# Performance work log

Measured on AMD Instinct MI355X. Metric: run time of the kernel, lower is better.

Reference implementation:

```python
import jax, jax.numpy as jnp
import numpy as np

NUM_EMB = 8192
EMB_DIM = 1024
BETA = 0.25  # commitment_cost, legacy=True


def setup_inputs() -> dict:
    key = jax.random.key(0)
    k1, k2 = jax.random.split(key)
    z = jax.random.normal(k1, (8, EMB_DIM, 32, 32), dtype=jnp.float32)
    # torch: embedding.weight.data.uniform_(-1/num_embeddings, 1/num_embeddings)
    emb_weight = jax.random.uniform(
        k2, (NUM_EMB, EMB_DIM), dtype=jnp.float32,
        minval=-1.0 / NUM_EMB, maxval=1.0 / NUM_EMB)
    return {"z": z, "emb_weight": emb_weight}


def reference(z, emb_weight):
    B, C, H, W = z.shape
    # b c h w -> b h w c
    z_work = jnp.transpose(z, (0, 2, 3, 1))
    z_flat = z_work.reshape(-1, EMB_DIM)  # [N, D]
    # squared distances: |z|^2 + |e|^2 - 2 z e^T  -> [N, K]
    d = (jnp.sum(z_flat * z_flat, axis=1, keepdims=True)
         + jnp.sum(emb_weight * emb_weight, axis=1)
         - 2.0 * jnp.einsum('nd,kd->nk', z_flat, emb_weight))
    idx = jnp.argmin(d, axis=1)  # [N]
    # codebook gather
    z_q = emb_weight[idx].reshape(z_work.shape)
    # usage counts (bincount) -> perplexity (EMA buffers omitted: no effect on outputs)
    counts = jax.ops.segment_sum(jnp.ones_like(idx, dtype=jnp.float32), idx,
                                 num_segments=NUM_EMB)
    avg_probs = counts / jnp.maximum(counts.sum(), 1.0)
    perplexity = jnp.exp(-jnp.sum(avg_probs * jnp.log(avg_probs + 1e-10)))
    sg = jax.lax.stop_gradient
    # legacy loss: mean((sg(zq)-z)^2) + beta*mean((zq-sg(z))^2)
    loss = (jnp.mean((sg(z_q) - z_work) ** 2)
            + BETA * jnp.mean((z_q - sg(z_work)) ** 2))
    # straight-through estimator
    z_q_ste = z_work + sg(z_q - z_work)
    # b h w c -> b c h w
    z_q_out = jnp.transpose(z_q_ste, (0, 3, 1, 2))
    return z_q_out, loss, perplexity, idx
```

## Files before the change

### kernel.cpp

```cpp
#include <hip/hip_runtime.h>
#include <math.h>

#define NROWS 8192
#define KCODES 8192
#define DDIM 1024
#define ZQ_ELEMS 8388608

typedef int i4 __attribute__((ext_vector_type(4)));

#define W0_QZ8     0u
#define W0_QE8     8388608u
#define W0_SZ      16777216u
#define W0_SE      16809984u
#define W0_CAND    16842752u
#define W0_CVAL    18939904u
#define W0_CCNT    23134208u
#define W0_COUNTS  23166976u
#define W0_ZNORM   23199744u
#define W0_ROWMIN  23232512u
#define W0_NEED    23265280u
#define W1_CAND    0u
#define W1_CVAL    2097152u
#define W1_CCNT    6291456u
#define W1_COUNTS  6324224u
#define W1_ZNORM   6356992u
#define W1_ROWMIN  6389760u
#define W1_NEED    6422528u
#define W3_CAND    0u
#define W3_CCNT    2097152u
#define W3_COUNTS  2129920u
#define W3_ZNORM   2162688u
#define W3_ROWMIN  2195456u
#define W3_NEED    2228224u

#define CAP 128
#define MARGIN  7.5e-4f
#define MARGIN2 6e-4f

typedef __attribute__((address_space(3))) unsigned int lds_u32;
typedef __attribute__((address_space(1))) const unsigned int glb_u32;
static __device__ __forceinline__ void glds16(const void* g, void* l) {
    __builtin_amdgcn_global_load_lds((glb_u32*)g, (lds_u32*)l, 16, 0, 0);
}

__global__ __launch_bounds__(256) void prep_kernel(const float* __restrict__ z,
                                                   const float* __restrict__ emb,
                                                   char* __restrict__ qz8,
                                                   char* __restrict__ qe8,
                                                   float* __restrict__ sz,
                                                   float* __restrict__ se,
                                                   float* __restrict__ zT,
                                                   float* __restrict__ zn,
                                                   unsigned int* __restrict__ ccnt,
                                                   float* __restrict__ counts,
                                                   int* __restrict__ rowming,
                                                   float* __restrict__ outbuf) {
    int blk = blockIdx.x;
    int t = threadIdx.x;
    if (blk >= 256) {
        __shared__ float wm[4];
        int k0 = (blk - 256) * 2;
        int half = t >> 7;
        int li = t & 127;
        int row = k0 + half;
        const float* er = emb + (size_t)row * 1024 + li * 8;
        float4 v0 = *(const float4*)er;
        float4 v1 = *(const float4*)(er + 4);
        float lm = fmaxf(fmaxf(fmaxf(fabsf(v0.x), fabsf(v0.y)), fmaxf(fabsf(v0.z), fabsf(v0.w))),
                         fmaxf(fmaxf(fabsf(v1.x), fabsf(v1.y)), fmaxf(fabsf(v1.z), fabsf(v1.w))));
#pragma unroll
        for (int off = 32; off; off >>= 1) lm = fmaxf(lm, __shfl_down(lm, off, 64));
        int w = t >> 6;
        if ((t & 63) == 0) wm[w] = lm;
        __syncthreads();
        float rmax = fmaxf(wm[half * 2], wm[half * 2 + 1]);
        float inv = rmax > 0.f ? 127.f / rmax : 0.f;
        int q0 = (int)rintf(v0.x * inv), q1 = (int)rintf(v0.y * inv);
        int q2 = (int)rintf(v0.z * inv), q3 = (int)rintf(v0.w * inv);
        int q4 = (int)rintf(v1.x * inv), q5 = (int)rintf(v1.y * inv);
        int q6 = (int)rintf(v1.z * inv), q7 = (int)rintf(v1.w * inv);
        uint2 o;
        o.x = (q0 & 255) | ((q1 & 255) << 8) | ((q2 & 255) << 16) | ((unsigned)(q3 & 255) << 24);
        o.y = (q4 & 255) | ((q5 & 255) << 8) | ((q6 & 255) << 16) | ((unsigned)(q7 & 255) << 24);
        *(uint2*)(qe8 + (size_t)row * 1024 + li * 8) = o;
        if (li == 0) se[row] = rmax * (1.f / 127.f);
        return;
    }
    if (t < 32) {
        int i = blk * 32 + t;
        ccnt[i] = 0u;
        counts[i] = 0.f;
        rowming[i] = 0x7f7f7f7f;
    }
    if (blk == 0 && t == 32) outbuf[ZQ_ELEMS] = 0.f;

    __shared__ float T[32 * 33];
    __shared__ double D[32 * 32];
    __shared__ float mxa[32 * 8];
    __shared__ float invS[32];
    int b = blk >> 5, ht = blk & 31;
    int hw0 = ht * 32;
    int dsub = t >> 3, hseg = (t & 7) * 4;
    int hsub = dsub, dd = hseg;
    double a0 = 0.0, a1 = 0.0, a2 = 0.0, a3 = 0.0;
    float lmax = 0.f;
    for (int dt = 0; dt < 32; ++dt) {
        int d0 = dt * 32;
        float4 v = *(const float4*)(z + (size_t)b * 1048576 + (size_t)(d0 + dsub) * 1024 + hw0 + hseg);
        a0 += (double)v.x * v.x;
        a1 += (double)v.y * v.y;
        a2 += (double)v.z * v.z;
        a3 += (double)v.w * v.w;
        T[dsub * 33 + hseg + 0] = v.x;
        T[dsub * 33 + hseg + 1] = v.y;
        T[dsub * 33 + hseg + 2] = v.z;
        T[dsub * 33 + hseg + 3] = v.w;
        __syncthreads();
        float t0 = T[(dd + 0) * 33 + hsub];
        float t1 = T[(dd + 1) * 33 + hsub];
        float t2 = T[(dd + 2) * 33 + hsub];
        float t3 = T[(dd + 3) * 33 + hsub];
        if (zT) {
            float4 o4; o4.x = t0; o4.y = t1; o4.z = t2; o4.w = t3;
            *(float4*)(zT + ((size_t)(b * 1024 + hw0 + hsub) << 10) + d0 + dd) = o4;
        }
        lmax = fmaxf(lmax, fmaxf(fmaxf(fabsf(t0), fabsf(t1)), fmaxf(fabsf(t2), fabsf(t3))));
        __syncthreads();
    }
    D[dsub * 32 + hseg + 0] = a0;
    D[dsub * 32 + hseg + 1] = a1;
    D[dsub * 32 + hseg + 2] = a2;
    D[dsub * 32 + hseg + 3] = a3;
    mxa[hsub * 8 + (t & 7)] = lmax;
    __syncthreads();
    if (t < 32) {
        double s = 0.0;
        for (int i = 0; i < 32; ++i) s += D[i * 32 + t];
        zn[b * 1024 + hw0 + t] = (float)s;
        float rm = 0.f;
#pragma unroll
        for (int j = 0; j < 8; ++j) rm = fmaxf(rm, mxa[t * 8 + j]);
        sz[b * 1024 + hw0 + t] = rm * (1.f / 127.f);
        invS[t] = rm > 0.f ? 127.f / rm : 0.f;
    }
    __syncthreads();
    if (zT) {
        int row = t >> 3;
        int dseg = (t & 7) * 128;
        float inv = invS[row];
        const float4* zr = (const float4*)(zT + ((size_t)(b * 1024 + hw0 + row) << 10) + dseg);
        int* qo = (int*)(qz8 + ((size_t)(b * 1024 + hw0 + row) << 10) + dseg);
#pragma unroll 8
        for (int jj = 0; jj < 32; ++jj) {
            float4 v = zr[jj];
            int q0 = (int)rintf(v.x * inv), q1 = (int)rintf(v.y * inv);
            int q2 = (int)rintf(v.z * inv), q3 = (int)rintf(v.w * inv);
            qo[jj] = (q0 & 255) | ((q1 & 255) << 8) | ((q2 & 255) << 16) | ((unsigned)(q3 & 255) << 24);
        }
    } else {
        for (int dt = 0; dt < 32; ++dt) {
            int d0 = dt * 32;
            float4 v = *(const float4*)(z + (size_t)b * 1048576 + (size_t)(d0 + dsub) * 1024 + hw0 + hseg);
            T[dsub * 33 + hseg + 0] = v.x;
            T[dsub * 33 + hseg + 1] = v.y;
            T[dsub * 33 + hseg + 2] = v.z;
            T[dsub * 33 + hseg + 3] = v.w;
            __syncthreads();
            float inv = invS[hsub];
            int q0 = (int)rintf(T[(dd + 0) * 33 + hsub] * inv);
            int q1 = (int)rintf(T[(dd + 1) * 33 + hsub] * inv);
            int q2 = (int)rintf(T[(dd + 2) * 33 + hsub] * inv);
            int q3 = (int)rintf(T[(dd + 3) * 33 + hsub] * inv);
            int packed = (q0 & 255) | ((q1 & 255) << 8) | ((q2 & 255) << 16) | ((unsigned)(q3 & 255) << 24);
            *(int*)(qz8 + ((size_t)(b * 1024 + hw0 + hsub) << 10) + d0 + dd) = packed;
            __syncthreads();
        }
    }
}

__global__ __launch_bounds__(256) void znorm_kernel(const float* __restrict__ z,
                                                    float* __restrict__ zn) {
    int b = blockIdx.x >> 2;
    int hw = (blockIdx.x & 3) * 256 + threadIdx.x;
    const float* base = z + (size_t)b * 1048576 + hw;
    double s = 0.0;
#pragma unroll 16
    for (int d = 0; d < DDIM; ++d) {
        float v = base[(size_t)d * 1024];
        s += (double)v * (double)v;
    }
    zn[b * 1024 + hw] = (float)s;
}

__global__ __launch_bounds__(256, 4) void stage1_kernel(const char* __restrict__ qz,
                                                        const char* __restrict__ qe,
                                                        const float* __restrict__ sz,
                                                        const float* __restrict__ se,
                                                        unsigned short* __restrict__ cand,
                                                        float* __restrict__ cval,
                                                        unsigned int* __restrict__ ccnt,
                                                        int* __restrict__ rowming) {
    __shared__ char As[128 * 128];
    __shared__ char Bs[128 * 128];
    __shared__ int rowminS[128];
    __shared__ float szS[128], seS[128];

    int t = threadIdx.x;
    int w = t >> 6, lane = t & 63;
    int q = lane >> 4, l15 = lane & 15;
    int wr = (w >> 1) * 64, wc = (w & 1) * 64;
    int n0 = blockIdx.x * 128;
    int k0 = blockIdx.y * 128;
    if (t < 128) {
        rowminS[t] = 0x7f7f7f7f;
        szS[t] = sz[n0 + t];
        seS[t] = se[k0 + t];
    }

    const char* gA[4];
    const char* gB[4];
    {
        int rsub = lane >> 3;
        int clog = (lane & 7) ^ (rsub & 7);
#pragma unroll
        for (int c = 0; c < 4; ++c) {
            int cc = w * 4 + c;
            int r = cc * 8 + rsub;
            gA[c] = qz + ((size_t)(n0 + r) << 10) + clog * 16;
            gB[c] = qe + ((size_t)(k0 + r) << 10) + clog * 16;
        }
    }
    int Aoff[4][2], Boff[4][2];
#pragma unroll
    for (int rf = 0; rf < 4; ++rf) {
#pragma unroll
        for (int ks = 0; ks < 2; ++ks) {
            int r = wr + rf * 16 + l15;
            Aoff[rf][ks] = r * 128 + (((ks * 4 + q) ^ (r & 7)) * 16);
            int rb = wc + rf * 16 + l15;
            Boff[rf][ks] = rb * 128 + (((ks * 4 + q) ^ (rb & 7)) * 16);
        }
    }

    i4 acc[4][4];
    const i4 z4 = {0, 0, 0, 0};
#pragma unroll
    for (int rf = 0; rf < 4; ++rf)
#pragma unroll
        for (int cf = 0; cf < 4; ++cf) acc[rf][cf] = z4;

    for (int s = 0; s < 8; ++s) {
        __syncthreads();
#pragma unroll
        for (int c = 0; c < 4; ++c) {
            int cc = w * 4 + c;
            glds16(gA[c], As + cc * 1024);
            glds16(gB[c], Bs + cc * 1024);
            gA[c] += 128;
            gB[c] += 128;
        }
        __syncthreads();
#pragma unroll
        for (int ks = 0; ks < 2; ++ks) {
            i4 af[4], bf[4];
#pragma unroll
            for (int rf = 0; rf < 4; ++rf) af[rf] = *(const i4*)(As + Aoff[rf][ks]);
#pragma unroll
            for (int cf = 0; cf < 4; ++cf) bf[cf] = *(const i4*)(Bs + Boff[cf][ks]);
#pragma unroll
            for (int rf = 0; rf < 4; ++rf)
#pragma unroll
                for (int cf = 0; cf < 4; ++cf)
                    acc[rf][cf] = __builtin_amdgcn_mfma_i32_16x16x64_i8(af[rf], bf[cf], acc[rf][cf], 0, 0, 0);
        }
    }

#pragma unroll
    for (int rf = 0; rf < 4; ++rf) {
#pragma unroll
        for (int reg = 0; reg < 4; ++reg) {
            int r = wr + rf * 16 + q * 4 + reg;
            float zs = szS[r];
            float m4 = INFINITY;
#pragma unroll
            for (int cf = 0; cf < 4; ++cf) {
                float s1 = 16.0f - 2.0f * (float)acc[rf][cf][reg] * (zs * seS[wc + cf * 16 + l15]);
                m4 = fminf(m4, s1);
            }
            m4 = fminf(m4, __shfl_xor(m4, 1, 16));
            m4 = fminf(m4, __shfl_xor(m4, 2, 16));
            m4 = fminf(m4, __shfl_xor(m4, 4, 16));
            m4 = fminf(m4, __shfl_xor(m4, 8, 16));
            if (l15 == 0) atomicMin(&rowminS[r], __float_as_int(m4));
        }
    }
    __syncthreads();
    if (t < 128) {
        int mine = rowminS[t];
        int gold = atomicMin(&rowming[n0 + t], mine);
        rowminS[t] = gold < mine ? gold : mine;
    }
    __syncthreads();
#pragma unroll
    for (int rf = 0; rf < 4; ++rf) {
#pragma unroll
        for (int reg = 0; reg < 4; ++reg) {
            int r = wr + rf * 16 + q * 4 + reg;
            float zs = szS[r];
            float rm = __int_as_float(rowminS[r]) + MARGIN;
#pragma unroll
            for (int cf = 0; cf < 4; ++cf) {
                float s1 = 16.0f - 2.0f * (float)acc[rf][cf][reg] * (zs * seS[wc + cf * 16 + l15]);
                if (s1 <= rm) {
                    int kg = k0 + wc + cf * 16 + l15;
                    unsigned pos = atomicAdd(&ccnt[n0 + r], 1u);
                    if (pos < CAP) {
                        cand[(size_t)(n0 + r) * CAP + pos] = (unsigned short)kg;
                        if (cval) cval[(size_t)(n0 + r) * CAP + pos] = s1;
                    }
                }
            }
        }
    }
}

__global__ __launch_bounds__(256) void stage2_kernel(const float* __restrict__ z,
                                                     const float* __restrict__ zT,
                                                     const float* __restrict__ emb,
                                                     const unsigned short* __restrict__ cand,
                                                     const float* __restrict__ cval,
                                                     const unsigned int* __restrict__ ccnt,
                                                     const float* __restrict__ zn,
                                                     float* __restrict__ counts,
                                                     float* __restrict__ outbuf) {
    int t = threadIdx.x;
    int w = t >> 6, lane = t & 63;
    int n = blockIdx.x * 4 + w;
    unsigned cnt = ccnt[n];
    float Zn = zn[n];
    float thr = INFINITY;

    if (cval && cnt <= CAP) {
        const float* cv = cval + (size_t)n * CAP;
        float v0 = (unsigned)lane < cnt ? cv[lane] : INFINITY;
        float v1 = (unsigned)(64 + lane) < cnt ? cv[64 + lane] : INFINITY;
        float m = fminf(v0, v1);
#pragma unroll
        for (int off = 32; off; off >>= 1) m = fminf(m, __shfl_xor(m, off, 64));
        thr = m + MARGIN2;
        unsigned long long m0 = __ballot(v0 <= thr);
        unsigned long long m1 = __ballot(v1 <= thr);
        if (__popcll(m0) + __popcll(m1) == 1) {
            if (lane == 0) {
                int slot = m0 ? ((int)__ffsll((unsigned long long)m0) - 1)
                              : 64 + ((int)__ffsll((unsigned long long)m1) - 1);
                int K = cand[(size_t)n * CAP + slot];
                outbuf[ZQ_ELEMS + 2 + n] = (float)K;
                atomicAdd(&counts[K], 1.0f);
            }
            return;
        }
    }
    float4 zreg[4];
    if (zT) {
        const float4* zr = (const float4*)(zT + ((size_t)n << 10));
#pragma unroll
        for (int i = 0; i < 4; ++i) zreg[i] = zr[lane + i * 64];
    } else {
        int b = n >> 10, hw = n & 1023;
        const float* zb = z + (size_t)b * 1048576 + hw;
#pragma unroll
        for (int i = 0; i < 4; ++i) {
            int e = (lane + i * 64) * 4;
            zreg[i].x = zb[(size_t)(e + 0) << 10];
            zreg[i].y = zb[(size_t)(e + 1) << 10];
            zreg[i].z = zb[(size_t)(e + 2) << 10];
            zreg[i].w = zb[(size_t)(e + 3) << 10];
        }
    }
    float bs = INFINITY;
    int bk = 0x7fffffff;
    if (cnt <= CAP) {
        for (unsigned c = 0; c < cnt; ++c) {
            if (cval && cval[(size_t)n * CAP + c] > thr) continue;
            int k = cand[(size_t)n * CAP + c];
            const float4* e4 = (const float4*)(emb + (size_t)k * 1024);
            double pd = 0.0;
#pragma unroll
            for (int i = 0; i < 4; ++i) {
                float4 e = e4[lane + i * 64];
                float4 zv = zreg[i];
                float p = (zv.x * e.x + zv.y * e.y) + (zv.z * e.z + zv.w * e.w);
                pd += (double)p;
            }
#pragma unroll
            for (int off = 32; off; off >>= 1) pd += __shfl_down(pd, off, 64);
            if (lane == 0) {
                float s = Zn - 2.0f * (float)pd;
                if (s < bs || (s == bs && k < bk)) { bs = s; bk = k; }
            }
        }
    } else {
        for (int k = 0; k < KCODES; ++k) {
            const float4* e4 = (const float4*)(emb + (size_t)k * 1024);
            double pd = 0.0;
#pragma unroll
            for (int i = 0; i < 4; ++i) {
                float4 e = e4[lane + i * 64];
                float4 zv = zreg[i];
                float p = (zv.x * e.x + zv.y * e.y) + (zv.z * e.z + zv.w * e.w);
                pd += (double)p;
            }
#pragma unroll
            for (int off = 32; off; off >>= 1) pd += __shfl_down(pd, off, 64);
            if (lane == 0) {
                float s = Zn - 2.0f * (float)pd;
                if (s < bs || (s == bs && k < bk)) { bs = s; bk = k; }
            }
        }
    }
    if (lane == 0) {
        outbuf[ZQ_ELEMS + 2 + n] = (float)bk;
        atomicAdd(&counts[bk], 1.0f);
    }
}

__global__ __launch_bounds__(1024) void perp_kernel(const float* __restrict__ counts,
                                                    float* __restrict__ outbuf) {
    __shared__ double sh[16];
    int tid = threadIdx.x;
    double h = 0.0;
    for (int i = tid; i < KCODES; i += 1024) {
        float c = counts[i];
        float p = c * (1.0f / 8192.0f);
        h += (double)(p * logf(p + 1e-10f));
    }
#pragma unroll
    for (int off = 32; off; off >>= 1) h += __shfl_down(h, off, 64);
    if ((tid & 63) == 0) sh[tid >> 6] = h;
    __syncthreads();
    if (tid == 0) {
        double H = 0.0;
#pragma unroll
        for (int i = 0; i < 16; ++i) H += sh[i];
        outbuf[ZQ_ELEMS + 1] = (float)exp(-H);
    }
}

__global__ __launch_bounds__(256) void gather_kernel(const float* __restrict__ z,
                                                     const float* __restrict__ emb,
                                                     const float* __restrict__ counts,
                                                     float* __restrict__ outbuf) {
    __shared__ float E[64 * 65];
    __shared__ int idxs[64];
    __shared__ float lsh[4];
    int blk = blockIdx.x;
    int ct = blk & 15;
    int hwt = (blk >> 4) & 15;
    int b = blk >> 8;
    int c0 = ct * 64;
    int n0 = b * 1024 + hwt * 64;
    int tid = threadIdx.x;
    if (tid < 64) idxs[tid] = (int)outbuf[ZQ_ELEMS + 2 + n0 + tid];
    __syncthreads();
    {
        int i0 = tid >> 4;
        int cc4 = (tid & 15) * 4;
#pragma unroll
        for (int rep = 0; rep < 4; ++rep) {
            int i = i0 + rep * 16;
            float4 v = *(const float4*)(emb + (size_t)idxs[i] * DDIM + c0 + cc4);
            E[i * 65 + cc4 + 0] = v.x;
            E[i * 65 + cc4 + 1] = v.y;
            E[i * 65 + cc4 + 2] = v.z;
            E[i * 65 + cc4 + 3] = v.w;
        }
    }
    __syncthreads();
    float ls = 0.f;
    int hwl = tid & 63;
    int cb = tid >> 6;
    size_t obase = (size_t)b * 1048576 + (size_t)hwt * 64 + hwl;
#pragma unroll
    for (int rep = 0; rep < 16; ++rep) {
        int cc = cb + rep * 4;
        size_t off = obase + (size_t)(c0 + cc) * 1024;
        float zv = z[off];
        float e = E[hwl * 65 + cc];
        float d = e - zv;
        outbuf[off] = zv + d;
        ls += d * d;
    }
#pragma unroll
    for (int off = 32; off; off >>= 1) ls += __shfl_down(ls, off, 64);
    if ((tid & 63) == 0) lsh[tid >> 6] = ls;
    __syncthreads();
    if (tid == 0) {
        float bsum = lsh[0] + lsh[1] + lsh[2] + lsh[3];
        atomicAdd(&outbuf[ZQ_ELEMS], bsum * (1.25f / 8388608.0f));
    }
    if (counts && blk == 0) {
        __shared__ double psh[4];
        double h = 0.0;
        for (int i = tid; i < KCODES; i += 256) {
            float c = counts[i];
            float p = c * (1.0f / 8192.0f);
            h += (double)(p * logf(p + 1e-10f));
        }
#pragma unroll
        for (int off = 32; off; off >>= 1) h += __shfl_down(h, off, 64);
        if ((tid & 63) == 0) psh[tid >> 6] = h;
        __syncthreads();
        if (tid == 0)
            outbuf[ZQ_ELEMS + 1] = (float)exp(-(psh[0] + psh[1] + psh[2] + psh[3]));
    }
}

#define SC_PMIN   0
#define SC_PIDX   65536
#define SC_ENORM  131072
#define SC_COUNTS 139264
#define SC_ZNORM  147456

__global__ __launch_bounds__(256) void enorm_kernel(const float* __restrict__ emb,
                                                    float* __restrict__ outbuf) {
    int wave = threadIdx.x >> 6;
    int lane = threadIdx.x & 63;
    int k = blockIdx.x * 4 + wave;
    const float4* row = (const float4*)(emb + (size_t)k * DDIM);
    float s = 0.f;
#pragma unroll
    for (int j = 0; j < 4; ++j) {
        float4 v = row[lane + 64 * j];
        s += v.x * v.x + v.y * v.y + v.z * v.z + v.w * v.w;
    }
#pragma unroll
    for (int off = 32; off; off >>= 1) s += __shfl_down(s, off, 64);
    if (lane == 0) outbuf[SC_ENORM + k] = s;
}

#define BD 32
#define LDT 68
__global__ __launch_bounds__(256) void argmin_kernel(const float* __restrict__ z,
                                                     const float* __restrict__ emb,
                                                     float* __restrict__ outbuf) {
    __shared__ float Asf[BD * LDT];
    __shared__ float Bsf[BD * LDT];
    __shared__ float redV[64 * 17];
    __shared__ float redI[64 * 17];
    int tid = threadIdx.x;
    int tx = tid & 15, ty = tid >> 4;
    int n0 = blockIdx.x * 64;
    int b = n0 >> 10, hw0 = n0 & 1023;
    const float* zbase = z + (size_t)b * 1048576 + hw0;
    int kChunk0 = blockIdx.y * 1024;
    float Zn[4];
#pragma unroll
    for (int i = 0; i < 4; ++i) Zn[i] = outbuf[SC_ZNORM + n0 + 4 * tx + i];
    float bestV[4] = {INFINITY, INFINITY, INFINITY, INFINITY};
    int bestI[4] = {0, 0, 0, 0};
    for (int kt = 0; kt < 16; ++kt) {
        int k0 = kChunk0 + kt * 64;
        double acc64[4][4] = {};
        for (int d0 = 0; d0 < DDIM; d0 += BD) {
            {
                int r4 = (tid & 15) * 4, ddA = tid >> 4;
#pragma unroll
                for (int rep = 0; rep < 2; ++rep) {
                    int dd = ddA + rep * 16;
                    float4 v = *(const float4*)(zbase + (size_t)(d0 + dd) * 1024 + r4);
                    *(float4*)(&Asf[dd * LDT + r4]) = v;
                }
            }
            {
                int dd4 = (tid & 7) * 4, kkB = tid >> 3;
#pragma unroll
                for (int rep = 0; rep < 2; ++rep) {
                    int kk = kkB + rep * 32;
                    float4 v = *(const float4*)(emb + (size_t)(k0 + kk) * DDIM + d0 + dd4);
                    Bsf[(dd4 + 0) * LDT + kk] = v.x;
                    Bsf[(dd4 + 1) * LDT + kk] = v.y;
                    Bsf[(dd4 + 2) * LDT + kk] = v.z;
                    Bsf[(dd4 + 3) * LDT + kk] = v.w;
                }
            }
            __syncthreads();
            float acc[4][4] = {};
#pragma unroll
            for (int dd = 0; dd < BD; ++dd) {
                float4 a = *(const float4*)(&Asf[dd * LDT + 4 * tx]);
                float4 bv = *(const float4*)(&Bsf[dd * LDT + 4 * ty]);
                float ar[4] = {a.x, a.y, a.z, a.w};
                float br[4] = {bv.x, bv.y, bv.z, bv.w};
#pragma unroll
                for (int i = 0; i < 4; ++i)
#pragma unroll
                    for (int j = 0; j < 4; ++j) acc[i][j] += ar[i] * br[j];
            }
            __syncthreads();
#pragma unroll
            for (int i = 0; i < 4; ++i)
#pragma unroll
                for (int j = 0; j < 4; ++j) acc64[i][j] += (double)acc[i][j];
        }
#pragma unroll
        for (int j = 0; j < 4; ++j) {
            int k = k0 + 4 * ty + j;
            float en = outbuf[SC_ENORM + k];
#pragma unroll
            for (int i = 0; i < 4; ++i) {
                float dotf = (float)acc64[i][j];
                float tt = Zn[i] + en;
                float s = tt - 2.0f * dotf;
                if (s < bestV[i]) { bestV[i] = s; bestI[i] = k; }
            }
        }
    }
#pragma unroll
    for (int i = 0; i < 4; ++i) {
        redV[(4 * tx + i) * 17 + ty] = bestV[i];
        redI[(4 * tx + i) * 17 + ty] = (float)bestI[i];
    }
    __syncthreads();
    if (tid < 64) {
        float bv = INFINITY;
        int bi = 0x7fffffff;
        for (int tt = 0; tt < 16; ++tt) {
            float v = redV[tid * 17 + tt];
            int ix = (int)redI[tid * 17 + tt];
            if (v < bv || (v == bv && ix < bi)) { bv = v; bi = ix; }
        }
        int n = n0 + tid;
        outbuf[SC_PMIN + n * 8 + blockIdx.y] = bv;
        outbuf[SC_PIDX + n * 8 + blockIdx.y] = (float)bi;
    }
}

__global__ __launch_bounds__(256) void reduce_kernel(float* __restrict__ outbuf) {
    int n = blockIdx.x * 256 + threadIdx.x;
    float bv = INFINITY;
    int bi = 0x7fffffff;
#pragma unroll
    for (int c = 0; c < 8; ++c) {
        float v = outbuf[SC_PMIN + n * 8 + c];
        int ix = (int)outbuf[SC_PIDX + n * 8 + c];
        if (v < bv || (v == bv && ix < bi)) { bv = v; bi = ix; }
    }
    outbuf[ZQ_ELEMS + 2 + n] = (float)bi;
    atomicAdd(&outbuf[SC_COUNTS + bi], 1.0f);
}

extern "C" void kernel_launch(void* const* d_in, const int* in_sizes, int n_in,
                              void* d_out, int out_size, void* d_ws, size_t ws_size,
                              hipStream_t stream) {
    const float* z = (const float*)d_in[0];
    const float* emb = (const float*)d_in[1];
    float* out = (float*)d_out;
    unsigned char* ws = (unsigned char*)d_ws;
    (void)in_sizes; (void)n_in; (void)out_size;

    if (ws_size >= (size_t)W0_NEED) {
        char* qz8 = (char*)(ws + W0_QZ8);
        char* qe8 = (char*)(ws + W0_QE8);
        float* sz = (float*)(ws + W0_SZ);
        float* se = (float*)(ws + W0_SE);
        unsigned short* cand = (unsigned short*)(ws + W0_CAND);
        float* cval = (float*)(ws + W0_CVAL);
        unsigned int* ccnt = (unsigned int*)(ws + W0_CCNT);
        float* counts = (float*)(ws + W0_COUNTS);
        float* zn = (float*)(ws + W0_ZNORM);
        int* rowming = (int*)(ws + W0_ROWMIN);
        float* zT = out;

        prep_kernel<<<4352, 256, 0, stream>>>(z, emb, qz8, qe8, sz, se, zT, zn, ccnt, counts, rowming, out);
        stage1_kernel<<<dim3(64, 64), 256, 0, stream>>>(qz8, qe8, sz, se, cand, cval, ccnt, rowming);
        stage2_kernel<<<2048, 256, 0, stream>>>(z, zT, emb, cand, cval, ccnt, zn, counts, out);
        gather_kernel<<<2048, 256, 0, stream>>>(z, emb, counts, out);
    } else if (ws_size >= (size_t)W1_NEED) {
        char* qz8 = (char*)out;
        char* qe8 = (char*)out + 8388608;
        float* sz = out + 4194304;
        float* se = out + 4202496;
        unsigned short* cand = (unsigned short*)(ws + W1_CAND);
        float* cval = (float*)(ws + W1_CVAL);
        unsigned int* ccnt = (unsigned int*)(ws + W1_CCNT);
        float* counts = (float*)(ws + W1_COUNTS);
        float* zn = (float*)(ws + W1_ZNORM);
        int* rowming = (int*)(ws + W1_ROWMIN);

        prep_kernel<<<4352, 256, 0, stream>>>(z, emb, qz8, qe8, sz, se, (float*)nullptr, zn, ccnt, counts, rowming, out);
        stage1_kernel<<<dim3(64, 64), 256, 0, stream>>>(qz8, qe8, sz, se, cand, cval, ccnt, rowming);
        stage2_kernel<<<2048, 256, 0, stream>>>(z, (const float*)nullptr, emb, cand, cval, ccnt, zn, counts, out);
        gather_kernel<<<2048, 256, 0, stream>>>(z, emb, counts, out);
    } else if (ws_size >= (size_t)W3_NEED) {
        char* qz8 = (char*)out;
        char* qe8 = (char*)out + 8388608;
        float* sz = out + 4194304;
        float* se = out + 4202496;
        unsigned short* cand = (unsigned short*)(ws + W3_CAND);
        unsigned int* ccnt = (unsigned int*)(ws + W3_CCNT);
        float* counts = (float*)(ws + W3_COUNTS);
        float* zn = (float*)(ws + W3_ZNORM);
        int* rowming = (int*)(ws + W3_ROWMIN);

        prep_kernel<<<4352, 256, 0, stream>>>(z, emb, qz8, qe8, sz, se, (float*)nullptr, zn, ccnt, counts, rowming, out);
        stage1_kernel<<<dim3(64, 64), 256, 0, stream>>>(qz8, qe8, sz, se, cand, (float*)nullptr, ccnt, rowming);
        stage2_kernel<<<2048, 256, 0, stream>>>(z, (const float*)nullptr, emb, cand,
                                                (const float*)nullptr, ccnt, zn, counts, out);
        gather_kernel<<<2048, 256, 0, stream>>>(z, emb, counts, out);
    } else {
        hipMemsetAsync(out + SC_COUNTS, 0, KCODES * sizeof(float), stream);
        hipMemsetAsync(out + ZQ_ELEMS, 0, sizeof(float), stream);
        enorm_kernel<<<2048, 256, 0, stream>>>(emb, out);
        znorm_kernel<<<32, 256, 0, stream>>>(z, out + SC_ZNORM);
        argmin_kernel<<<dim3(128, 8), 256, 0, stream>>>(z, emb, out);
        reduce_kernel<<<32, 256, 0, stream>>>(out);
        perp_kernel<<<1, 1024, 0, stream>>>(out + SC_COUNTS, out);
        gather_kernel<<<2048, 256, 0, stream>>>(z, emb, (const float*)nullptr, out);
    }
}
```

Before: 286.7 us.

## Split z-transpose prep into 512 smaller blocks with double-buffered LDS tile

Measured after the change: 282.1 us. No clear change (-1.6%).

```diff
diff --git a/kernel.cpp b/kernel.cpp
--- a/kernel.cpp
+++ b/kernel.cpp
@@ -57,9 +57,9 @@
                                                    float* __restrict__ outbuf) {
     int blk = blockIdx.x;
     int t = threadIdx.x;
-    if (blk >= 256) {
+    if (blk >= 512) {
         __shared__ float wm[4];
-        int k0 = (blk - 256) * 2;
+        int k0 = (blk - 512) * 2;
         int half = t >> 7;
         int li = t & 127;
         int row = k0 + half;
@@ -86,7 +86,7 @@
         if (li == 0) se[row] = rmax * (1.f / 127.f);
         return;
     }
-    if (t < 32) {
+    if (blk < 256 && t < 32) {
         int i = blk * 32 + t;
         ccnt[i] = 0u;
         counts[i] = 0.f;
@@ -94,86 +94,79 @@
     }
     if (blk == 0 && t == 32) outbuf[ZQ_ELEMS] = 0.f;
 
-    __shared__ float T[32 * 33];
-    __shared__ double D[32 * 32];
-    __shared__ float mxa[32 * 8];
-    __shared__ float invS[32];
-    int b = blk >> 5, ht = blk & 31;
-    int hw0 = ht * 32;
-    int dsub = t >> 3, hseg = (t & 7) * 4;
-    int hsub = dsub, dd = hseg;
-    double a0 = 0.0, a1 = 0.0, a2 = 0.0, a3 = 0.0;
+    __shared__ float T[2][64 * 17];
+    __shared__ float invS[16];
+    int b = blk >> 6;
+    int hw0 = (blk & 63) * 16;
+    int dsub = t >> 2, hseg = (t & 3) * 4;
+    int hsub = t >> 4, ddg = (t & 15) * 4;
+    double acc = 0.0;
     float lmax = 0.f;
-    for (int dt = 0; dt < 32; ++dt) {
-        int d0 = dt * 32;
+    int p = 0;
+    for (int dt = 0; dt < 16; ++dt) {
+        int d0 = dt * 64;
         float4 v = *(const float4*)(z + (size_t)b * 1048576 + (size_t)(d0 + dsub) * 1024 + hw0 + hseg);
-        a0 += (double)v.x * v.x;
-        a1 += (double)v.y * v.y;
-        a2 += (double)v.z * v.z;
-        a3 += (double)v.w * v.w;
-        T[dsub * 33 + hseg + 0] = v.x;
-        T[dsub * 33 + hseg + 1] = v.y;
-        T[dsub * 33 + hseg + 2] = v.z;
-        T[dsub * 33 + hseg + 3] = v.w;
+        float* Tp = T[p];
+        Tp[dsub * 17 + hseg + 0] = v.x;
+        Tp[dsub * 17 + hseg + 1] = v.y;
+        Tp[dsub * 17 + hseg + 2] = v.z;
+        Tp[dsub * 17 + hseg + 3] = v.w;
         __syncthreads();
-        float t0 = T[(dd + 0) * 33 + hsub];
-        float t1 = T[(dd + 1) * 33 + hsub];
-        float t2 = T[(dd + 2) * 33 + hsub];
-        float t3 = T[(dd + 3) * 33 + hsub];
+        float t0 = Tp[(ddg + 0) * 17 + hsub];
+        float t1 = Tp[(ddg + 1) * 17 + hsub];
+        float t2 = Tp[(ddg + 2) * 17 + hsub];
+        float t3 = Tp[(ddg + 3) * 17 + hsub];
         if (zT) {
             float4 o4; o4.x = t0; o4.y = t1; o4.z = t2; o4.w = t3;
-            *(float4*)(zT + ((size_t)(b * 1024 + hw0 + hsub) << 10) + d0 + dd) = o4;
-        }
+            *(float4*)(zT + ((size_t)(b * 1024 + hw0 + hsub) << 10) + d0 + ddg) = o4;
+        }
+        acc += (double)t0 * t0 + (double)t1 * t1 + (double)t2 * t2 + (double)t3 * t3;
         lmax = fmaxf(lmax, fmaxf(fmaxf(fabsf(t0), fabsf(t1)), fmaxf(fabsf(t2), fabsf(t3))));
-        __syncthreads();
-    }
-    D[dsub * 32 + hseg + 0] = a0;
-    D[dsub * 32 + hseg + 1] = a1;
-    D[dsub * 32 + hseg + 2] = a2;
-    D[dsub * 32 + hseg + 3] = a3;
-    mxa[hsub * 8 + (t & 7)] = lmax;
-    __syncthreads();
-    if (t < 32) {
-        double s = 0.0;
-        for (int i = 0; i < 32; ++i) s += D[i * 32 + t];
-        zn[b * 1024 + hw0 + t] = (float)s;
-        float rm = 0.f;
-#pragma unroll
-        for (int j = 0; j < 8; ++j) rm = fmaxf(rm, mxa[t * 8 + j]);
-        sz[b * 1024 + hw0 + t] = rm * (1.f / 127.f);
-        invS[t] = rm > 0.f ? 127.f / rm : 0.f;
+        p ^= 1;
+    }
+#pragma unroll
+    for (int m = 8; m; m >>= 1) {
+        acc += __shfl_xor(acc, m, 16);
+        lmax = fmaxf(lmax, __shfl_xor(lmax, m, 16));
+    }
+    if ((t & 15) == 0) {
+        zn[b * 1024 + hw0 + hsub] = (float)acc;
+        sz[b * 1024 + hw0 + hsub] = lmax * (1.f / 127.f);
+        invS[hsub] = lmax > 0.f ? 127.f / lmax : 0.f;
     }
     __syncthreads();
     if (zT) {
-        int row = t >> 3;
-        int dseg = (t & 7) * 128;
+        int row = t >> 4;
+        int seg = t & 15;
         float inv = invS[row];
-        const float4* zr = (const float4*)(zT + ((size_t)(b * 1024 + hw0 + row) << 10) + dseg);
-        int* qo = (int*)(qz8 + ((size_t)(b * 1024 + hw0 + row) << 10) + dseg);
-#pragma unroll 8
-        for (int jj = 0; jj < 32; ++jj) {
+        const float4* zr = (const float4*)(zT + ((size_t)(b * 1024 + hw0 + row) << 10)) + seg * 16;
+        int* qo = (int*)(qz8 + ((size_t)(b * 1024 + hw0 + row) << 10)) + seg * 16;
+#pragma unroll 4
+        for (int jj = 0; jj < 16; ++jj) {
             float4 v = zr[jj];
             int q0 = (int)rintf(v.x * inv), q1 = (int)rintf(v.y * inv);
             int q2 = (int)rintf(v.z * inv), q3 = (int)rintf(v.w * inv);
             qo[jj] = (q0 & 255) | ((q1 & 255) << 8) | ((q2 & 255) << 16) | ((unsigned)(q3 & 255) << 24);
         }
     } else {
-        for (int dt = 0; dt < 32; ++dt) {
-            int d0 = dt * 32;
+        p = 0;
+        for (int dt = 0; dt < 16; ++dt) {
+            int d0 = dt * 64;
             float4 v = *(const float4*)(z + (size_t)b * 1048576 + (size_t)(d0 + dsub) * 1024 + hw0 + hseg);
-            T[dsub * 33 + hseg + 0] = v.x;
-            T[dsub * 33 + hseg + 1] = v.y;
-            T[dsub * 33 + hseg + 2] = v.z;
-            T[dsub * 33 + hseg + 3] = v.w;
+            float* Tp = T[p];
+            Tp[dsub * 17 + hseg + 0] = v.x;
+            Tp[dsub * 17 + hseg + 1] = v.y;
+            Tp[dsub * 17 + hseg + 2] = v.z;
+            Tp[dsub * 17 + hseg + 3] = v.w;
             __syncthreads();
             float inv = invS[hsub];
-            int q0 = (int)rintf(T[(dd + 0) * 33 + hsub] * inv);
-            int q1 = (int)rintf(T[(dd + 1) * 33 + hsub] * inv);
-            int q2 = (int)rintf(T[(dd + 2) * 33 + hsub] * inv);
-            int q3 = (int)rintf(T[(dd + 3) * 33 + hsub] * inv);
-            int packed = (q0 & 255) | ((q1 & 255) << 8) | ((q2 & 255) << 16) | ((unsigned)(q3 & 255) << 24);
-            *(int*)(qz8 + ((size_t)(b * 1024 + hw0 + hsub) << 10) + d0 + dd) = packed;
-            __syncthreads();
+            int q0 = (int)rintf(Tp[(ddg + 0) * 17 + hsub] * inv);
+            int q1 = (int)rintf(Tp[(ddg + 1) * 17 + hsub] * inv);
+            int q2 = (int)rintf(Tp[(ddg + 2) * 17 + hsub] * inv);
+            int q3 = (int)rintf(Tp[(ddg + 3) * 17 + hsub] * inv);
+            *(int*)(qz8 + ((size_t)(b * 1024 + hw0 + hsub) << 10) + d0 + ddg) =
+                (q0 & 255) | ((q1 & 255) << 8) | ((q2 & 255) << 16) | ((unsigned)(q3 & 255) << 24);
+            p ^= 1;
         }
     }
 }
@@ -672,7 +665,7 @@
         int* rowming = (int*)(ws + W0_ROWMIN);
         float* zT = out;
 
-        prep_kernel<<<4352, 256, 0, stream>>>(z, emb, qz8, qe8, sz, se, zT, zn, ccnt, counts, rowming, out);
+        prep_kernel<<<4608, 256, 0, stream>>>(z, emb, qz8, qe8, sz, se, zT, zn, ccnt, counts, rowming, out);
         stage1_kernel<<<dim3(64, 64), 256, 0, stream>>>(qz8, qe8, sz, se, cand, cval, ccnt, rowming);
         stage2_kernel<<<2048, 256, 0, stream>>>(z, zT, emb, cand, cval, ccnt, zn, counts, out);
         gather_kernel<<<2048, 256, 0, stream>>>(z, emb, counts, out);
@@ -688,7 +681,7 @@
         float* zn = (float*)(ws + W1_ZNORM);
         int* rowming = (int*)(ws + W1_ROWMIN);
 
-        prep_kernel<<<4352, 256, 0, stream>>>(z, emb, qz8, qe8, sz, se, (float*)nullptr, zn, ccnt, counts, rowming, out);
+        prep_kernel<<<4608, 256, 0, stream>>>(z, emb, qz8, qe8, sz, se, (float*)nullptr, zn, ccnt, counts, rowming, out);
         stage1_kernel<<<dim3(64, 64), 256, 0, stream>>>(qz8, qe8, sz, se, cand, cval, ccnt, rowming);
         stage2_kernel<<<2048, 256, 0, stream>>>(z, (const float*)nullptr, emb, cand, cval, ccnt, zn, counts, out);
         gather_kernel<<<2048, 256, 0, stream>>>(z, emb, counts, out);
@@ -703,7 +696,7 @@
         float* zn = (float*)(ws + W3_ZNORM);
         int* rowming = (int*)(ws + W3_ROWMIN);
 
-        prep_kernel<<<4352, 256, 0, stream>>>(z, emb, qz8, qe8, sz, se, (float*)nullptr, zn, ccnt, counts, rowming, out);
+        prep_kernel<<<4608, 256, 0, stream>>>(z, emb, qz8, qe8, sz, se, (float*)nullptr, zn, ccnt, counts, rowming, out);
         stage1_kernel<<<dim3(64, 64), 256, 0, stream>>>(qz8, qe8, sz, se, cand, (float*)nullptr, ccnt, rowming);
         stage2_kernel<<<2048, 256, 0, stream>>>(z, (const float*)nullptr, emb, cand,
                                                 (const float*)nullptr, ccnt, zn, counts, out);
```
